# Performance work log

Hardware: AMD Instinct MI355X
Metric: run time of the kernel (lower is better)

Reference implementation:

```python
import jax, jax.numpy as jnp
import numpy as np

N = 20000       # nodes
E = 320000      # edges (before self-loops)
F_IN = 1024     # num_features
H = 4           # head_num
C = 64          # hidden_size
NC = 4          # n_classes
NEG_SLOPE = 0.2 # PyG GATConv default


def setup_inputs() -> dict:
    key = jax.random.key(0)
    ks = jax.random.split(key, 16)
    def w(k, shape, fan_in):
        return jax.random.normal(k, shape, dtype=jnp.float32) / np.sqrt(fan_in)
    x = jax.random.normal(ks[0], (N, F_IN), dtype=jnp.float32)
    edge_index = jax.random.randint(ks[1], (2, E), 0, N, dtype=jnp.int64)
    return {
        "x": x,
        "edge_index": edge_index,
        # layer 1: F_IN -> H*C, concat
        "w1": w(ks[2], (F_IN, H * C), F_IN),
        "as1": w(ks[3], (H, C), C),
        "ad1": w(ks[4], (H, C), C),
        "b1": jnp.zeros((H * C,), jnp.float32),
        # layer 2: H*C -> H*C, concat
        "w2": w(ks[5], (H * C, H * C), H * C),
        "as2": w(ks[6], (H, C), C),
        "ad2": w(ks[7], (H, C), C),
        "b2": jnp.zeros((H * C,), jnp.float32),
        # out layer: H*C -> C, 1 head, concat=False
        "w3": w(ks[8], (H * C, 1 * C), H * C),
        "as3": w(ks[9], (1, C), C),
        "ad3": w(ks[10], (1, C), C),
        "b3": jnp.zeros((C,), jnp.float32),
        # classifier
        "wc": w(ks[11], (C, NC), C),
        "bc": jnp.zeros((NC,), jnp.float32),
    }


def gat_layer(x, src, dst, W, a_src, a_dst, bias, concat):
    """PyG GATConv (eval mode, self-loops already added to src/dst)."""
    n = x.shape[0]
    Hh, Cc = a_src.shape
    h = (x @ W).reshape(n, Hh, Cc)                       # [N,H,C]
    al_s = jnp.sum(h * a_src[None], axis=-1)             # [N,H]
    al_d = jnp.sum(h * a_dst[None], axis=-1)             # [N,H]
    e = al_s[src] + al_d[dst]                            # [E,H]
    e = jax.nn.leaky_relu(e, NEG_SLOPE)
    # segment softmax over incoming edges of each destination node
    emax = jax.ops.segment_max(e, dst, num_segments=n)   # [N,H]
    ex = jnp.exp(e - emax[dst])
    denom = jax.ops.segment_sum(ex, dst, num_segments=n) # [N,H]
    alpha = ex / (denom[dst] + 1e-16)                    # [E,H]
    msg = h[src] * alpha[..., None]                      # [E,H,C]
    out = jax.ops.segment_sum(msg, dst, num_segments=n)  # [N,H,C]
    if concat:
        out = out.reshape(n, Hh * Cc)
    else:
        out = out.mean(axis=1)
    return out + bias


def reference(x, edge_index, w1, as1, ad1, b1, w2, as2, ad2, b2,
              w3, as3, ad3, b3, wc, bc):
    n = x.shape[0]
    loop = jnp.arange(n, dtype=edge_index.dtype)
    src = jnp.concatenate([edge_index[0], loop])
    dst = jnp.concatenate([edge_index[1], loop])
    out = jax.nn.relu(gat_layer(x, src, dst, w1, as1, ad1, b1, True))
    out = jax.nn.relu(gat_layer(out, src, dst, w2, as2, ad2, b2, True))
    out = gat_layer(out, src, dst, w3, as3, ad3, b3, False)
    return out @ wc + bc                                  # [N, n_classes]
```

## Files before the change

kernel.cpp:

```cpp
#include <hip/hip_runtime.h>

#define N_NODES 20000
#define N_EDGES 320000
#define ET (N_EDGES + N_NODES)
#define F_IN 1024
#define HC 256
#define NC 4

typedef unsigned short ushort_t;
typedef __attribute__((ext_vector_type(8))) short short8;
typedef __attribute__((ext_vector_type(4))) float f32x4;

__device__ inline ushort_t f2bf(float f) {
    unsigned u = __float_as_uint(f);
    unsigned r = (u + 0x7fffu + ((u >> 16) & 1u)) >> 16;
    return (ushort_t)r;
}
__device__ inline float bf2f(ushort_t u) {
    return __uint_as_float(((unsigned)u) << 16);
}

__device__ inline unsigned cvt_pk_bf16(float lo, float hi) {
    unsigned r;
    asm("v_cvt_pk_bf16_f32 %0, %1, %2" : "=v"(r) : "v"(lo), "v"(hi));
    return r;
}

#define GLOAD16(gp, lp) __builtin_amdgcn_global_load_lds( \
    (const __attribute__((address_space(1))) void*)(gp),  \
    (__attribute__((address_space(3))) void*)(lp), 16, 0, 0)

__global__ void count_kernel(const int* __restrict__ ei, int* __restrict__ counts) {
    int e = blockIdx.x * blockDim.x + threadIdx.x;
    if (e >= ET) return;
    int dst = (e < N_EDGES) ? ei[N_EDGES + e] : (e - N_EDGES);
    atomicAdd(&counts[dst], 1);
}

__global__ void scan_kernel(const int* __restrict__ counts, int* __restrict__ row_ptr,
                            int* __restrict__ cursor) {
    __shared__ int sums[1024];
    int t = threadIdx.x;
    const int per = (N_NODES + 1023) / 1024;
    int b = t * per;
    int e = min(b + per, N_NODES);
    int s = 0;
    for (int i = b; i < e; ++i) s += counts[i];
    sums[t] = s;
    __syncthreads();
    for (int off = 1; off < 1024; off <<= 1) {
        int v = (t >= off) ? sums[t - off] : 0;
        __syncthreads();
        sums[t] += v;
        __syncthreads();
    }
    int run = (t == 0) ? 0 : sums[t - 1];
    for (int i = b; i < e; ++i) {
        row_ptr[i] = run;
        cursor[i]  = run;
        run += counts[i];
    }
    if (t == 0) row_ptr[N_NODES] = ET;
}

__global__ void scatter_kernel(const int* __restrict__ ei, int* __restrict__ cursor,
                               int* __restrict__ col) {
    int e = blockIdx.x * blockDim.x + threadIdx.x;
    if (e >= ET) return;
    int src, dst;
    if (e < N_EDGES) { src = ei[e]; dst = ei[N_EDGES + e]; }
    else             { src = dst = e - N_EDGES; }
    int pos = atomicAdd(&cursor[dst], 1);
    col[pos] = src;
}

__global__ void split_T(const float* __restrict__ in, ushort_t* __restrict__ hi,
                        ushort_t* __restrict__ lo, int K, int Nn) {
    int idx = blockIdx.x * blockDim.x + threadIdx.x;
    if (idx >= K * Nn) return;
    int k = idx / Nn, n = idx - k * Nn;
    float v = in[idx];
    ushort_t h = f2bf(v);
    hi[(size_t)n * K + k] = h;
    lo[(size_t)n * K + k] = f2bf(v - bf2f(h));
}

#define AL_EPILOGUE()                                                              \
    {                                                                              \
        float asv[NF], adv[NF];                                                    \
        _Pragma("unroll")                                                          \
        for (int j = 0; j < NF; ++j) {                                             \
            int col = bn + wn * SN + j * 16 + (lane & 15);                         \
            asv[j] = as_w[col];                                                    \
            adv[j] = ad_w[col];                                                    \
        }                                                                          \
        float* s_as = (float*)smem;                                   \
        float* s_ad = (float*)smem + 2 * BM;                                       \
        _Pragma("unroll")                                                          \
        for (int i = 0; i < MF; ++i) {                                             \
            _Pragma("unroll")                                                      \
            for (int rr = 0; rr < 4; ++rr) {                                       \
                float ps = 0.f, pd = 0.f;                                          \
                _Pragma("unroll")                                                  \
                for (int j = 0; j < NF; ++j) {                                     \
                    ps += acc[i][j][rr] * asv[j];                                  \
                    pd += acc[i][j][rr] * adv[j];                                  \
                }                                                                  \
                _Pragma("unroll")                                                  \
                for (int o = 1; o < 16; o <<= 1) {                                 \
                    ps += __shfl_xor(ps, o, 64);                                   \
                    pd += __shfl_xor(pd, o, 64);                                   \
                }                                                                  \
                if ((lane & 15) == 0) {                                            \
                    int rl = wm * SM + i * 16 + (lane >> 4) * 4 + rr;              \
                    s_as[wn * BM + rl] = ps;                                       \
                    s_ad[wn * BM + rl] = pd;                                       \
                }                                                                  \
            }                                                                      \
        }                                                                          \
        __syncthreads();                                                           \
        if (t < BM) {                                                              \
            int row = bm + t;                                                      \
            if (row < M) {                                                         \
                int hb = bn >> 6;                                                  \
                als[row * H + hb] = s_as[t] + s_as[BM + t];                        \
                ald[row * H + hb] = s_ad[t] + s_ad[BM + t];                        \
            }                                                                      \
        }                                                                          \
    }

template<int GY>
__launch_bounds__(256)
__global__ void gemm_f32a_ks(const float* __restrict__ X,
                             const ushort_t* __restrict__ BTh, const ushort_t* __restrict__ BTl,
                             float* __restrict__ Cp0, float* __restrict__ Cp1,
                             int M, int K, int NT) {
    constexpr int BM = 128, BN = 64, SM = 64, SN = 32, MF = 4, NF = 2;
    __shared__ __align__(16) char smem[49152];

    const int t = threadIdx.x, lane = t & 63, w = t >> 6;
    const int wm = w >> 1, wn = w & 1;
    const int nwg = gridDim.x;
    const int id = blockIdx.x;
    const int q = nwg >> 3, r = nwg & 7;
    const int xcd = id & 7, idx = id >> 3;
    const int logical = (xcd < r ? xcd * (q + 1) : r * (q + 1) + (xcd - r) * q) + idx;
    const int nwg_half = nwg >> 1;
    const int ks = logical / nwg_half;
    const int rem = logical - ks * nwg_half;
    const int bm = (rem / GY) * BM, bn = (rem % GY) * BN;
    const int kbase = ks * (K >> 1);
    float* Cp = ks ? Cp1 : Cp0;

    const int achk = lane & 3;
    const float* xRow[2]; int aoff[2];
    #pragma unroll
    for (int qq = 0; qq < 2; ++qq) {
        int arow = (w * 2 + qq) * 16 + (lane >> 2);
        int grow = min(bm + arow, M - 1);
        xRow[qq] = X + (size_t)grow * K + kbase + achk * 8;
        aoff[qq] = arow * 64 + ((achk ^ ((arow >> 1) & 3)) * 16);
    }
    const int gchunk = ((lane & 3) ^ ((lane >> 3) & 3)) * 16;
    const int brow = w * 16 + (lane >> 2);
    const size_t gB = (size_t)(bn + brow) * K * 2 + (size_t)kbase * 2 + gchunk;
    const int lB = w * 1024;

    const char* Bhb = (const char*)BTh;
    const char* Blb = (const char*)BTl;
    const int c16 = (lane >> 4);
    const int NTs = K >> 7;

    f32x4 acc[MF][NF];
    #pragma unroll
    for (int i = 0; i < MF; ++i)
        #pragma unroll
        for (int j = 0; j < NF; ++j) acc[i][j] = (f32x4){0.f, 0.f, 0.f, 0.f};

    float4 cur0[2][2], cur1[2][2], nxt0[2][2], nxt1[2][2];
    #pragma unroll
    for (int qq = 0; qq < 2; ++qq)
        #pragma unroll
        for (int kc = 0; kc < 2; ++kc) {
            cur0[qq][kc] = *(const float4*)(xRow[qq] + kc * 32);
            cur1[qq][kc] = *(const float4*)(xRow[qq] + kc * 32 + 4);
        }

    for (int ts = 0; ts < NTs; ++ts) {
        size_t kb = (size_t)ts * 128;
        #pragma unroll
        for (int kc = 0; kc < 2; ++kc) {
            GLOAD16(Bhb + gB + kb + kc * 64, smem + 32768 + kc * 4096 + lB);
            GLOAD16(Blb + gB + kb + kc * 64, smem + 40960 + kc * 4096 + lB);
        }
        if (ts + 1 < NTs) {
            #pragma unroll
            for (int qq = 0; qq < 2; ++qq)
                #pragma unroll
                for (int kc = 0; kc < 2; ++kc) {
                    nxt0[qq][kc] = *(const float4*)(xRow[qq] + (ts + 1) * 64 + kc * 32);
                    nxt1[qq][kc] = *(const float4*)(xRow[qq] + (ts + 1) * 64 + kc * 32 + 4);
                }
        }
        #pragma unroll
        for (int qq = 0; qq < 2; ++qq)
            #pragma unroll
            for (int kc = 0; kc < 2; ++kc) {
                float vv[8] = {cur0[qq][kc].x, cur0[qq][kc].y, cur0[qq][kc].z, cur0[qq][kc].w,
                               cur1[qq][kc].x, cur1[qq][kc].y, cur1[qq][kc].z, cur1[qq][kc].w};
                unsigned hp[4], lp[4];
                #pragma unroll
                for (int j = 0; j < 4; ++j) {
                    unsigned h = cvt_pk_bf16(vv[2 * j], vv[2 * j + 1]);
                    float h0 = __uint_as_float(h << 16);
                    float h1 = __uint_as_float(h & 0xFFFF0000u);
                    hp[j] = h;
                    lp[j] = cvt_pk_bf16(vv[2 * j] - h0, vv[2 * j + 1] - h1);
                }
                *(uint4*)(smem + kc * 8192 + aoff[qq])         = make_uint4(hp[0], hp[1], hp[2], hp[3]);
                *(uint4*)(smem + 16384 + kc * 8192 + aoff[qq]) = make_uint4(lp[0], lp[1], lp[2], lp[3]);
            }
        __syncthreads();
        #pragma unroll
        for (int kc = 0; kc < 2; ++kc) {
            short8 afh[MF], afl[MF], bfh[NF], bfl[NF];
            #pragma unroll
            for (int i = 0; i < MF; ++i) {
                int row = wm * SM + i * 16 + (lane & 15);
                int off = row * 64 + ((c16 ^ ((row >> 1) & 3)) * 16);
                afh[i] = *(const short8*)(smem + kc * 8192 + off);
                afl[i] = *(const short8*)(smem + 16384 + kc * 8192 + off);
            }
            #pragma unroll
            for (int j = 0; j < NF; ++j) {
                int row = wn * SN + j * 16 + (lane & 15);
                int off = row * 64 + ((c16 ^ ((row >> 1) & 3)) * 16);
                bfh[j] = *(const short8*)(smem + 32768 + kc * 4096 + off);
                bfl[j] = *(const short8*)(smem + 40960 + kc * 4096 + off);
            }
            #pragma unroll
            for (int i = 0; i < MF; ++i)
                #pragma unroll
                for (int j = 0; j < NF; ++j) {
                    acc[i][j] = __builtin_amdgcn_mfma_f32_16x16x32_bf16(afh[i], bfh[j], acc[i][j], 0, 0, 0);
                    acc[i][j] = __builtin_amdgcn_mfma_f32_16x16x32_bf16(afh[i], bfl[j], acc[i][j], 0, 0, 0);
                    acc[i][j] = __builtin_amdgcn_mfma_f32_16x16x32_bf16(afl[i], bfh[j], acc[i][j], 0, 0, 0);
                }
        }
        __syncthreads();
        #pragma unroll
        for (int qq = 0; qq < 2; ++qq)
            #pragma unroll
            for (int kc = 0; kc < 2; ++kc) { cur0[qq][kc] = nxt0[qq][kc]; cur1[qq][kc] = nxt1[qq][kc]; }
    }
    #pragma unroll
    for (int i = 0; i < MF; ++i) {
        int rbase = bm + wm * SM + i * 16 + (lane >> 4) * 4;
        #pragma unroll
        for (int j = 0; j < NF; ++j) {
            int col = bn + wn * SN + j * 16 + (lane & 15);
            #pragma unroll
            for (int rr = 0; rr < 4; ++rr)
                if (rbase + rr < M) Cp[(size_t)(rbase + rr) * NT + col] = acc[i][j][rr];
        }
    }
}

__launch_bounds__(256)
__global__ void reduce_al(float* __restrict__ B0, const float* __restrict__ Cp1,
                          const float* __restrict__ as_w, const float* __restrict__ ad_w,
                          float* __restrict__ als, float* __restrict__ ald) {
    int lane = threadIdx.x & 63, w = threadIdx.x >> 6;
    int row = blockIdx.x * 4 + w;
    if (row >= N_NODES) return;
    size_t base = (size_t)row * HC + lane * 4;
    float4 p0 = *(const float4*)&B0[base];
    float4 p1 = *(const float4*)&Cp1[base];
    float4 s = make_float4(p0.x + p1.x, p0.y + p1.y, p0.z + p1.z, p0.w + p1.w);
    *(float4*)&B0[base] = s;
    int head = lane >> 4;
    int cw = (lane & 15) * 4;
    float ps = s.x * as_w[head * 64 + cw + 0] + s.y * as_w[head * 64 + cw + 1]
             + s.z * as_w[head * 64 + cw + 2] + s.w * as_w[head * 64 + cw + 3];
    float pd = s.x * ad_w[head * 64 + cw + 0] + s.y * ad_w[head * 64 + cw + 1]
             + s.z * ad_w[head * 64 + cw + 2] + s.w * ad_w[head * 64 + cw + 3];
    #pragma unroll
    for (int o = 1; o < 16; o <<= 1) {
        ps += __shfl_xor(ps, o, 64);
        pd += __shfl_xor(pd, o, 64);
    }
    if ((lane & 15) == 0) {
        als[row * 4 + head] = ps;
        ald[row * 4 + head] = pd;
    }
}

template<int BMT, int GY, int H>
__launch_bounds__(256)
__global__ void gemm_mfma(const ushort_t* __restrict__ Ah, const ushort_t* __restrict__ Al,
                          const ushort_t* __restrict__ BTh, const ushort_t* __restrict__ BTl,
                          float* __restrict__ C, const float* __restrict__ as_w,
                          const float* __restrict__ ad_w, float* __restrict__ als,
                          float* __restrict__ ald, int M, int K, int NT) {
    constexpr int BM = BMT, BN = 64, SM = BM / 2, SN = 32, MF = SM / 16, NF = 2;
    constexpr int AQ = BM / 64;
    constexpr int ASZ = BM * 64;
    __shared__ __align__(16) char smem[4 * ASZ + 16384];

    const int t = threadIdx.x, lane = t & 63, w = t >> 6;
    const int wm = w >> 1, wn = w & 1;
    const int nwg = gridDim.x;
    const int id = blockIdx.x;
    const int q = nwg >> 3, r = nwg & 7;
    const int xcd = id & 7, idx = id >> 3;
    const int logical = (xcd < r ? xcd * (q + 1) : r * (q + 1) + (xcd - r) * q) + idx;
    const int bm = (logical / GY) * BM, bn = (logical % GY) * BN;
    const int gchunk = ((lane & 3) ^ ((lane >> 3) & 3)) * 16;

    size_t gA[AQ]; int lA[AQ];
    #pragma unroll
    for (int qq = 0; qq < AQ; ++qq) {
        int inst = w * AQ + qq;
        int arow = inst * 16 + (lane >> 2);
        int grow = min(bm + arow, M - 1);
        gA[qq] = (size_t)grow * K * 2 + gchunk;
        lA[qq] = inst * 1024;
    }
    const int brow = w * 16 + (lane >> 2);
    const size_t gB = (size_t)(bn + brow) * K * 2 + gchunk;
    const int lB = w * 1024;

    const char* Ahb = (const char*)Ah;
    const char* Alb = (const char*)Al;
    const char* Bhb = (const char*)BTh;
    const char* Blb = (const char*)BTl;
    const int c16 = (lane >> 4);
    const int NTs = K / 64;

    f32x4 acc[MF][NF];
    #pragma unroll
    for (int i = 0; i < MF; ++i)
        #pragma unroll
        for (int j = 0; j < NF; ++j) acc[i][j] = (f32x4){0.f, 0.f, 0.f, 0.f};

    for (int ts = 0; ts < NTs; ++ts) {
        size_t kb = (size_t)ts * 128;
        #pragma unroll
        for (int kc = 0; kc < 2; ++kc) {
            #pragma unroll
            for (int qq = 0; qq < AQ; ++qq) {
                GLOAD16(Ahb + gA[qq] + kb + kc * 64, smem + kc * ASZ + lA[qq]);
                GLOAD16(Alb + gA[qq] + kb + kc * 64, smem + 2 * ASZ + kc * ASZ + lA[qq]);
            }
            GLOAD16(Bhb + gB + kb + kc * 64, smem + 4 * ASZ + kc * 4096 + lB);
            GLOAD16(Blb + gB + kb + kc * 64, smem + 4 * ASZ + 8192 + kc * 4096 + lB);
        }
        __syncthreads();
        #pragma unroll
        for (int kc = 0; kc < 2; ++kc) {
            short8 afh[MF], afl[MF], bfh[NF], bfl[NF];
            #pragma unroll
            for (int i = 0; i < MF; ++i) {
                int row = wm * SM + i * 16 + (lane & 15);
                int off = row * 64 + ((c16 ^ ((row >> 1) & 3)) * 16);
                afh[i] = *(const short8*)(smem + kc * ASZ + off);
                afl[i] = *(const short8*)(smem + 2 * ASZ + kc * ASZ + off);
            }
            #pragma unroll
            for (int j = 0; j < NF; ++j) {
                int row = wn * SN + j * 16 + (lane & 15);
                int off = row * 64 + ((c16 ^ ((row >> 1) & 3)) * 16);
                bfh[j] = *(const short8*)(smem + 4 * ASZ + kc * 4096 + off);
                bfl[j] = *(const short8*)(smem + 4 * ASZ + 8192 + kc * 4096 + off);
            }
            #pragma unroll
            for (int i = 0; i < MF; ++i)
                #pragma unroll
                for (int j = 0; j < NF; ++j) {
                    acc[i][j] = __builtin_amdgcn_mfma_f32_16x16x32_bf16(afh[i], bfh[j], acc[i][j], 0, 0, 0);
                    acc[i][j] = __builtin_amdgcn_mfma_f32_16x16x32_bf16(afh[i], bfl[j], acc[i][j], 0, 0, 0);
                    acc[i][j] = __builtin_amdgcn_mfma_f32_16x16x32_bf16(afl[i], bfh[j], acc[i][j], 0, 0, 0);
                }
        }
        __syncthreads();
    }
    #pragma unroll
    for (int i = 0; i < MF; ++i) {
        int rbase = bm + wm * SM + i * 16 + (lane >> 4) * 4;
        #pragma unroll
        for (int j = 0; j < NF; ++j) {
            int col = bn + wn * SN + j * 16 + (lane & 15);
            #pragma unroll
            for (int rr = 0; rr < 4; ++rr)
                if (rbase + rr < M) C[(size_t)(rbase + rr) * NT + col] = acc[i][j][rr];
        }
    }
    AL_EPILOGUE()
}

template<int H>
__launch_bounds__(256)
__global__ void alpha_kernel(const float* __restrict__ als, const float* __restrict__ ald,
                             const int* __restrict__ row_ptr, const int* __restrict__ col,
                             float* __restrict__ alpha) {
    int lane = threadIdx.x & 63, w = threadIdx.x >> 6;
    int dst = blockIdx.x * 4 + w;
    if (dst >= N_NODES) return;
    int beg = row_ptr[dst], deg = row_ptr[dst + 1] - beg;
    constexpr int ES = 64 / H;
    int i_loc = lane / H, hh = lane % H;
    float ad = ald[dst * H + hh];
    float m = -1e30f, den = 0.f;
    for (int base = 0; base < deg; base += ES) {
        int i = base + i_loc;
        if (i < deg) {
            float e = als[col[beg + i] * H + hh] + ad;
            e = (e > 0.f) ? e : 0.2f * e;
            float nm = fmaxf(m, e);
            den = den * __expf(m - nm) + __expf(e - nm);
            m = nm;
        }
    }
    #pragma unroll
    for (int off = H; off < 64; off <<= 1) {
        float mo = __shfl_xor(m, off, 64);
        float dn = __shfl_xor(den, off, 64);
        float nm = fmaxf(m, mo);
        den = den * __expf(m - nm) + dn * __expf(mo - nm);
        m = nm;
    }
    float rden = 1.f / (den + 1e-16f);
    for (int base = 0; base < deg; base += ES) {
        int i = base + i_loc;
        if (i < deg) {
            float e = als[col[beg + i] * H + hh] + ad;
            e = (e > 0.f) ? e : 0.2f * e;
            alpha[(size_t)hh * ET + beg + i] = __expf(e - m) * rden;
        }
    }
}

template<int CT, int CW, int H, bool RELU, bool SPLIT, bool CLS>
__launch_bounds__(256)
__global__ void agg_v4(const float* __restrict__ h, const float* __restrict__ alpha,
                       const int* __restrict__ row_ptr, const int* __restrict__ col,
                       const float* __restrict__ bias,
                       ushort_t* __restrict__ oh, ushort_t* __restrict__ ol,
                       float* __restrict__ of,
                       const float* __restrict__ wc, const float* __restrict__ bc,
                       float* __restrict__ cls_out) {
    constexpr int NS  = CT / CW;
    constexpr int LPT = CW / 4;
    constexpr int TPW = 64 / LPT;
    static_assert(NS == H, "slice==head mapping");
    __shared__ int   s_src[4][64];
    __shared__ float s_alp[4][64];
    const int nwg = gridDim.x;
    const int q = nwg >> 3;
    int id = blockIdx.x;
    int logical = (id & 7) * q + (id >> 3);
    int slice = logical / (N_NODES / 4);
    int g = logical - slice * (N_NODES / 4);
    int lane = threadIdx.x & 63, w = threadIdx.x >> 6;
    int dst = g * 4 + w;
    int beg = row_ptr[dst], deg = row_ptr[dst + 1] - beg;
    int team = lane / LPT;
    int cc = (lane & (LPT - 1)) * 4;

    const int*   colP = col + beg;
    const float* aP   = alpha + (size_t)slice * ET + beg;
    const float* hS   = h + slice * CW + cc;

    float4 acc  = make_float4(0.f, 0.f, 0.f, 0.f);
    float4 acc2 = make_float4(0.f, 0.f, 0.f, 0.f);
    for (int base = 0; base < deg; base += 64) {
        int cnt = min(64, deg - base);
        if (lane < cnt) {
            s_src[w][lane] = colP[base + lane];
            s_alp[w][lane] = aP[base + lane];
        }
        int i = team;
        for (; i + TPW < cnt; i += 2 * TPW) {
            int   s0 = s_src[w][i],       s1 = s_src[w][i + TPW];
            float a0 = s_alp[w][i],       a1 = s_alp[w][i + TPW];
            float4 h0 = *(const float4*)&hS[s0 * CT];
            float4 h1 = *(const float4*)&hS[s1 * CT];
            acc.x  += a0 * h0.x; acc.y  += a0 * h0.y; acc.z  += a0 * h0.z; acc.w  += a0 * h0.w;
            acc2.x += a1 * h1.x; acc2.y += a1 * h1.y; acc2.z += a1 * h1.z; acc2.w += a1 * h1.w;
        }
        if (i < cnt) {
            int   s0 = s_src[w][i];
            float a0 = s_alp[w][i];
            float4 h0 = *(const float4*)&hS[s0 * CT];
            acc.x += a0 * h0.x; acc.y += a0 * h0.y; acc.z += a0 * h0.z; acc.w += a0 * h0.w;
        }
    }
    acc.x += acc2.x; acc.y += acc2.y; acc.z += acc2.z; acc.w += acc2.w;
    #pragma unroll
    for (int off = LPT; off < 64; off <<= 1) {
        acc.x += __shfl_xor(acc.x, off, 64);
        acc.y += __shfl_xor(acc.y, off, 64);
        acc.z += __shfl_xor(acc.z, off, 64);
        acc.w += __shfl_xor(acc.w, off, 64);
    }
    if (team == 0) {
        int ch = slice * CW + cc;
        float4 bv = *(const float4*)&bias[ch];
        float v0 = acc.x + bv.x, v1 = acc.y + bv.y, v2 = acc.z + bv.z, v3 = acc.w + bv.w;
        if (RELU) {
            v0 = fmaxf(v0, 0.f); v1 = fmaxf(v1, 0.f);
            v2 = fmaxf(v2, 0.f); v3 = fmaxf(v3, 0.f);
        }
        if (CLS) {
            float ps[NC];
            #pragma unroll
            for (int k = 0; k < NC; ++k)
                ps[k] = v0 * wc[(cc + 0) * NC + k] + v1 * wc[(cc + 1) * NC + k]
                      + v2 * wc[(cc + 2) * NC + k] + v3 * wc[(cc + 3) * NC + k];
            #pragma unroll
            for (int o = 1; o < 16; o <<= 1)
                #pragma unroll
                for (int k = 0; k < NC; ++k) ps[k] += __shfl_xor(ps[k], o, 64);
            if (lane == 0) {
                #pragma unroll
                for (int k = 0; k < NC; ++k) cls_out[(size_t)dst * NC + k] = ps[k] + bc[k];
            }
        } else {
            size_t idx = (size_t)dst * CT + ch;
            if (SPLIT) {
                ushort4 h4, l4;
                h4.x = f2bf(v0); l4.x = f2bf(v0 - bf2f(h4.x));
                h4.y = f2bf(v1); l4.y = f2bf(v1 - bf2f(h4.y));
                h4.z = f2bf(v2); l4.z = f2bf(v2 - bf2f(h4.z));
                h4.w = f2bf(v3); l4.w = f2bf(v3 - bf2f(h4.w));
                *(ushort4*)&oh[idx] = h4;
                *(ushort4*)&ol[idx] = l4;
            } else {
                *(float4*)&of[idx] = make_float4(v0, v1, v2, v3);
            }
        }
    }
}

extern "C" void kernel_launch(void* const* d_in, const int* in_sizes, int n_in,
                              void* d_out, int out_size, void* d_ws, size_t ws_size,
                              hipStream_t stream) {
    const float* x   = (const float*)d_in[0];
    const int*   ei  = (const int*)d_in[1];
    const float* w1  = (const float*)d_in[2];
    const float* as1 = (const float*)d_in[3];
    const float* ad1 = (const float*)d_in[4];
    const float* b1  = (const float*)d_in[5];
    const float* w2  = (const float*)d_in[6];
    const float* as2 = (const float*)d_in[7];
    const float* ad2 = (const float*)d_in[8];
    const float* b2  = (const float*)d_in[9];
    const float* w3  = (const float*)d_in[10];
    const float* as3 = (const float*)d_in[11];
    const float* ad3 = (const float*)d_in[12];
    const float* b3  = (const float*)d_in[13];
    const float* wc  = (const float*)d_in[14];
    const float* bc  = (const float*)d_in[15];
    float* out = (float*)d_out;

    char* ws = (char*)d_ws;
    size_t off = 0;
    auto alloc = [&](size_t bytes) -> char* {
        char* p = ws + off;
        off = (off + bytes + 255) & ~(size_t)255;
        return p;
    };

    int* counts  = (int*)alloc(N_NODES * 4);
    int* cursor  = (int*)alloc(N_NODES * 4);
    int* row_ptr = (int*)alloc((N_NODES + 1) * 4);
    int* colidx  = (int*)alloc(ET * 4);
    float* als   = (float*)alloc(N_NODES * 4 * 4);
    float* ald   = (float*)alloc(N_NODES * 4 * 4);
    float* alpha = (float*)alloc((size_t)4 * ET * 4);
    float* B0    = (float*)alloc((size_t)N_NODES * HC * 4);
    float* Cp1   = (float*)alloc((size_t)N_NODES * HC * 4);

    ushort_t* w1Th = (ushort_t*)alloc((size_t)F_IN * HC * 2);
    ushort_t* w1Tl = (ushort_t*)alloc((size_t)F_IN * HC * 2);
    ushort_t* w2Th = (ushort_t*)alloc((size_t)HC * HC * 2);
    ushort_t* w2Tl = (ushort_t*)alloc((size_t)HC * HC * 2);
    ushort_t* w3Th = (ushort_t*)alloc((size_t)HC * 64 * 2);
    ushort_t* w3Tl = (ushort_t*)alloc((size_t)HC * 64 * 2);
    ushort_t* B1h  = (ushort_t*)alloc((size_t)N_NODES * HC * 2);
    ushort_t* B1l  = (ushort_t*)alloc((size_t)N_NODES * HC * 2);

    hipMemsetAsync(counts, 0, N_NODES * sizeof(int), stream);
    int eb = (ET + 255) / 256;
    count_kernel<<<eb, 256, 0, stream>>>(ei, counts);
    scan_kernel<<<1, 1024, 0, stream>>>(counts, row_ptr, cursor);
    scatter_kernel<<<eb, 256, 0, stream>>>(ei, cursor, colidx);

    split_T<<<(F_IN * HC + 255) / 256, 256, 0, stream>>>(w1, w1Th, w1Tl, F_IN, HC);
    split_T<<<(HC * HC + 255) / 256, 256, 0, stream>>>(w2, w2Th, w2Tl, HC, HC);
    split_T<<<(HC * 64 + 255) / 256, 256, 0, stream>>>(w3, w3Th, w3Tl, HC, 64);

    const int nwg128 = ((N_NODES + 127) / 128) * (HC / 64);
    const int nblk_dst = N_NODES / 4;
    gemm_f32a_ks<4><<<2 * nwg128, 256, 0, stream>>>(x, w1Th, w1Tl, B0, Cp1, N_NODES, F_IN, HC);
    reduce_al<<<nblk_dst, 256, 0, stream>>>(B0, Cp1, as1, ad1, als, ald);
    alpha_kernel<4><<<nblk_dst, 256, 0, stream>>>(als, ald, row_ptr, colidx, alpha);
    agg_v4<256, 64, 4, true, true, false><<<4 * nblk_dst, 256, 0, stream>>>(
        B0, alpha, row_ptr, colidx, b1, B1h, B1l, nullptr, nullptr, nullptr, nullptr);
    gemm_mfma<128, 4, 4><<<nwg128, 256, 0, stream>>>(B1h, B1l, w2Th, w2Tl, B0, as2, ad2,
                                                     als, ald, N_NODES, HC, HC);
    alpha_kernel<4><<<nblk_dst, 256, 0, stream>>>(als, ald, row_ptr, colidx, alpha);
    agg_v4<256, 64, 4, true, true, false><<<4 * nblk_dst, 256, 0, stream>>>(
        B0, alpha, row_ptr, colidx, b2, B1h, B1l, nullptr, nullptr, nullptr, nullptr);
    const int nwg3 = (N_NODES + 63) / 64;
    gemm_mfma<64, 1, 1><<<nwg3, 256, 0, stream>>>(B1h, B1l, w3Th, w3Tl, B0, as3, ad3,
                                                  als, ald, N_NODES, HC, 64);
    alpha_kernel<1><<<nblk_dst, 256, 0, stream>>>(als, ald, row_ptr, colidx, alpha);
    agg_v4<64, 64, 1, false, false, true><<<nblk_dst, 256, 0, stream>>>(
        B0, alpha, row_ptr, colidx, b3, nullptr, nullptr, nullptr, wc, bc, out);
}
```

Baseline: 282.0 us.

## Replace direct global-to-LDS loads with register-staged prefetch in both GEMMs

Both GEMM kernels stop using global_load_lds for the B (and A) tiles. They now load the next k-step's tiles into registers right after the barrier and write them to swizzled LDS at the start of the following iteration. This overlaps global latency with the MFMA work of the current step, which the old synchronous LDS-direct loads could not do. The cost is extra VGPRs and explicit LDS stores, which may reduce occupancy.

```diff
diff --git a/kernel.cpp b/kernel.cpp
--- a/kernel.cpp
+++ b/kernel.cpp
@@ -25,10 +25,6 @@
     asm("v_cvt_pk_bf16_f32 %0, %1, %2" : "=v"(r) : "v"(lo), "v"(hi));
     return r;
 }
-
-#define GLOAD16(gp, lp) __builtin_amdgcn_global_load_lds( \
-    (const __attribute__((address_space(1))) void*)(gp),  \
-    (__attribute__((address_space(3))) void*)(lp), 16, 0, 0)
 
 __global__ void count_kernel(const int* __restrict__ ei, int* __restrict__ counts) {
     int e = blockIdx.x * blockDim.x + threadIdx.x;
@@ -161,13 +157,11 @@
         xRow[qq] = X + (size_t)grow * K + kbase + achk * 8;
         aoff[qq] = arow * 64 + ((achk ^ ((arow >> 1) & 3)) * 16);
     }
-    const int gchunk = ((lane & 3) ^ ((lane >> 3) & 3)) * 16;
     const int brow = w * 16 + (lane >> 2);
-    const size_t gB = (size_t)(bn + brow) * K * 2 + (size_t)kbase * 2 + gchunk;
-    const int lB = w * 1024;
-
-    const char* Bhb = (const char*)BTh;
-    const char* Blb = (const char*)BTl;
+    const ushort_t* BhP = BTh + (size_t)(bn + brow) * K + kbase + achk * 8;
+    const ushort_t* BlP = BTl + (size_t)(bn + brow) * K + kbase + achk * 8;
+    const int boff = brow * 64 + ((achk ^ ((brow >> 1) & 3)) * 16);
+
     const int c16 = (lane >> 4);
     const int NTs = K >> 7;
 
@@ -177,37 +171,28 @@
         #pragma unroll
         for (int j = 0; j < NF; ++j) acc[i][j] = (f32x4){0.f, 0.f, 0.f, 0.f};
 
-    float4 cur0[2][2], cur1[2][2], nxt0[2][2], nxt1[2][2];
+    float4 cA0[2][2], cA1[2][2];
+    uint4  cBh[2], cBl[2];
     #pragma unroll
     for (int qq = 0; qq < 2; ++qq)
         #pragma unroll
         for (int kc = 0; kc < 2; ++kc) {
-            cur0[qq][kc] = *(const float4*)(xRow[qq] + kc * 32);
-            cur1[qq][kc] = *(const float4*)(xRow[qq] + kc * 32 + 4);
-        }
+            cA0[qq][kc] = *(const float4*)(xRow[qq] + kc * 32);
+            cA1[qq][kc] = *(const float4*)(xRow[qq] + kc * 32 + 4);
+        }
+    #pragma unroll
+    for (int kc = 0; kc < 2; ++kc) {
+        cBh[kc] = *(const uint4*)(BhP + kc * 32);
+        cBl[kc] = *(const uint4*)(BlP + kc * 32);
+    }
 
     for (int ts = 0; ts < NTs; ++ts) {
-        size_t kb = (size_t)ts * 128;
-        #pragma unroll
-        for (int kc = 0; kc < 2; ++kc) {
-            GLOAD16(Bhb + gB + kb + kc * 64, smem + 32768 + kc * 4096 + lB);
-            GLOAD16(Blb + gB + kb + kc * 64, smem + 40960 + kc * 4096 + lB);
-        }
-        if (ts + 1 < NTs) {
-            #pragma unroll
-            for (int qq = 0; qq < 2; ++qq)
-                #pragma unroll
-                for (int kc = 0; kc < 2; ++kc) {
-                    nxt0[qq][kc] = *(const float4*)(xRow[qq] + (ts + 1) * 64 + kc * 32);
-                    nxt1[qq][kc] = *(const float4*)(xRow[qq] + (ts + 1) * 64 + kc * 32 + 4);
-                }
-        }
         #pragma unroll
         for (int qq = 0; qq < 2; ++qq)
             #pragma unroll
             for (int kc = 0; kc < 2; ++kc) {
-                float vv[8] = {cur0[qq][kc].x, cur0[qq][kc].y, cur0[qq][kc].z, cur0[qq][kc].w,
-                               cur1[qq][kc].x, cur1[qq][kc].y, cur1[qq][kc].z, cur1[qq][kc].w};
+                float vv[8] = {cA0[qq][kc].x, cA0[qq][kc].y, cA0[qq][kc].z, cA0[qq][kc].w,
+                               cA1[qq][kc].x, cA1[qq][kc].y, cA1[qq][kc].z, cA1[qq][kc].w};
                 unsigned hp[4], lp[4];
                 #pragma unroll
                 for (int j = 0; j < 4; ++j) {
@@ -220,7 +205,27 @@
                 *(uint4*)(smem + kc * 8192 + aoff[qq])         = make_uint4(hp[0], hp[1], hp[2], hp[3]);
                 *(uint4*)(smem + 16384 + kc * 8192 + aoff[qq]) = make_uint4(lp[0], lp[1], lp[2], lp[3]);
             }
+        #pragma unroll
+        for (int kc = 0; kc < 2; ++kc) {
+            *(uint4*)(smem + 32768 + kc * 4096 + boff) = cBh[kc];
+            *(uint4*)(smem + 40960 + kc * 4096 + boff) = cBl[kc];
+        }
         __syncthreads();
+        if (ts + 1 < NTs) {
+            int ko = (ts + 1) * 64;
+            #pragma unroll
+            for (int qq = 0; qq < 2; ++qq)
+                #pragma unroll
+                for (int kc = 0; kc < 2; ++kc) {
+                    cA0[qq][kc] = *(const float4*)(xRow[qq] + ko + kc * 32);
+                    cA1[qq][kc] = *(const float4*)(xRow[qq] + ko + kc * 32 + 4);
+                }
+            #pragma unroll
+            for (int kc = 0; kc < 2; ++kc) {
+                cBh[kc] = *(const uint4*)(BhP + ko + kc * 32);
+                cBl[kc] = *(const uint4*)(BlP + ko + kc * 32);
+            }
+        }
         #pragma unroll
         for (int kc = 0; kc < 2; ++kc) {
             short8 afh[MF], afl[MF], bfh[NF], bfl[NF];
@@ -248,10 +253,6 @@
                 }
         }
         __syncthreads();
-        #pragma unroll
-        for (int qq = 0; qq < 2; ++qq)
-            #pragma unroll
-            for (int kc = 0; kc < 2; ++kc) { cur0[qq][kc] = nxt0[qq][kc]; cur1[qq][kc] = nxt1[qq][kc]; }
     }
     #pragma unroll
     for (int i = 0; i < MF; ++i) {
@@ -315,25 +316,22 @@
     const int xcd = id & 7, idx = id >> 3;
     const int logical = (xcd < r ? xcd * (q + 1) : r * (q + 1) + (xcd - r) * q) + idx;
     const int bm = (logical / GY) * BM, bn = (logical % GY) * BN;
-    const int gchunk = ((lane & 3) ^ ((lane >> 3) & 3)) * 16;
-
-    size_t gA[AQ]; int lA[AQ];
+
+    const int achk = lane & 3;
+    const ushort_t* AhP[AQ]; const ushort_t* AlP[AQ]; int aoff[AQ];
     #pragma unroll
     for (int qq = 0; qq < AQ; ++qq) {
-        int inst = w * AQ + qq;
-        int arow = inst * 16 + (lane >> 2);
+        int arow = (w * AQ + qq) * 16 + (lane >> 2);
         int grow = min(bm + arow, M - 1);
-        gA[qq] = (size_t)grow * K * 2 + gchunk;
-        lA[qq] = inst * 1024;
+        AhP[qq] = Ah + (size_t)grow * K + achk * 8;
+        AlP[qq] = Al + (size_t)grow * K + achk * 8;
+        aoff[qq] = arow * 64 + ((achk ^ ((arow >> 1) & 3)) * 16);
     }
     const int brow = w * 16 + (lane >> 2);
-    const size_t gB = (size_t)(bn + brow) * K * 2 + gchunk;
-    const int lB = w * 1024;
-
-    const char* Ahb = (const char*)Ah;
-    const char* Alb = (const char*)Al;
-    const char* Bhb = (const char*)BTh;
-    const char* Blb = (const char*)BTl;
+    const ushort_t* BhP = BTh + (size_t)(bn + brow) * K + achk * 8;
+    const ushort_t* BlP = BTl + (size_t)(bn + brow) * K + achk * 8;
+    const int boff = brow * 64 + ((achk ^ ((brow >> 1) & 3)) * 16);
+
     const int c16 = (lane >> 4);
     const int NTs = K / 64;
 
@@ -343,19 +341,49 @@
         #pragma unroll
         for (int j = 0; j < NF; ++j) acc[i][j] = (f32x4){0.f, 0.f, 0.f, 0.f};
 
+    uint4 cAh[AQ][2], cAl[AQ][2], cBh[2], cBl[2];
+    #pragma unroll
+    for (int qq = 0; qq < AQ; ++qq)
+        #pragma unroll
+        for (int kc = 0; kc < 2; ++kc) {
+            cAh[qq][kc] = *(const uint4*)(AhP[qq] + kc * 32);
+            cAl[qq][kc] = *(const uint4*)(AlP[qq] + kc * 32);
+        }
+    #pragma unroll
+    for (int kc = 0; kc < 2; ++kc) {
+        cBh[kc] = *(const uint4*)(BhP + kc * 32);
+        cBl[kc] = *(const uint4*)(BlP + kc * 32);
+    }
+
     for (int ts = 0; ts < NTs; ++ts) {
-        size_t kb = (size_t)ts * 128;
+        #pragma unroll
+        for (int qq = 0; qq < AQ; ++qq)
+            #pragma unroll
+            for (int kc = 0; kc < 2; ++kc) {
+                *(uint4*)(smem + kc * ASZ + aoff[qq])           = cAh[qq][kc];
+                *(uint4*)(smem + 2 * ASZ + kc * ASZ + aoff[qq]) = cAl[qq][kc];
+            }
         #pragma unroll
         for (int kc = 0; kc < 2; ++kc) {
-            #pragma unroll
-            for (int qq = 0; qq < AQ; ++qq) {
-                GLOAD16(Ahb + gA[qq] + kb + kc * 64, smem + kc * ASZ + lA[qq]);
-                GLOAD16(Alb + gA[qq] + kb + kc * 64, smem + 2 * ASZ + kc * ASZ + lA[qq]);
-            }
-            GLOAD16(Bhb + gB + kb + kc * 64, smem + 4 * ASZ + kc * 4096 + lB);
-            GLOAD16(Blb + gB + kb + kc * 64, smem + 4 * ASZ + 8192 + kc * 4096 + lB);
+            *(uint4*)(smem + 4 * ASZ + kc * 4096 + boff)        = cBh[kc];
+            *(uint4*)(smem + 4 * ASZ + 8192 + kc * 4096 + boff) = cBl[kc];
         }
         __syncthreads();
+        if (ts + 1 < NTs) {
+            int ko = (ts + 1) * 64;
+            #pragma unroll
+            for (int qq = 0; qq < AQ; ++qq)
+                #pragma unroll
+                for (int kc = 0; kc < 2; ++kc) {
+                    cAh[qq][kc] = *(const uint4*)(AhP[qq] + ko + kc * 32);
+                    cAl[qq][kc] = *(const uint4*)(AlP[qq] + ko + kc * 32);
+                }
+            #pragma unroll
+            for (int kc = 0; kc < 2; ++kc) {
+                cBh[kc] = *(const uint4*)(BhP + ko + kc * 32);
+                cBl[kc] = *(const uint4*)(BlP + ko + kc * 32);
+            }
+        }
         #pragma unroll
         for (int kc = 0; kc < 2; ++kc) {
             short8 afh[MF], afl[MF], bfh[NF], bfl[NF];
```

Result: slower. 347.3 us (+23.2%).
